# Optimization experiments

Hardware: AMD Instinct MI355X
Metric: run time of the kernel (lower is better)

## Reference

```python
import jax, jax.numpy as jnp
import numpy as np


def setup_inputs() -> dict:
    key = jax.random.key(0)
    B, N = 4, 32768
    xyz = jax.random.normal(key, (B, N, 3), dtype=jnp.float32)
    return {"xyz": xyz, "K": 16, "nqueries": 2048}


def reference(xyz, K, nqueries):
    # xyz: (b, n, 3). Deterministic strided pick of nqueries query points
    # (stand-in for the KD-tree's distance-pick sampling), then brute-force KNN.
    b, n, _ = xyz.shape
    stride = n // nqueries
    q_idx = jnp.arange(nqueries) * stride          # (nq,)
    pts = xyz[:, q_idx, :]                          # (b, nq, 3) sampled query points
    # pairwise squared distances (b, nq, n)
    d = jnp.sum((pts[:, :, None, :] - xyz[:, None, :, :]) ** 2, axis=-1)
    _, idx = jax.lax.top_k(-d, K)                   # (b, nq, K) nearest-neighbor indices
    idx = idx.astype(jnp.int64)[..., None]          # (b, nq, K, 1) matches expand_dims(..., 3)
    return idx, pts
```

## Files before the change

kernel.cpp:

```cpp
#include <hip/hip_runtime.h>
#include <stdint.h>

#define NPTS  32768
#define NQ    2048
#define KNN   16
#define NB    4
#define TS    2048
#define BLOCK 512
#define WPB   8

__device__ __forceinline__ void insert_all(float d, int p, int lane, int t,
                                           float& ld, int& li, float& tau)
{
    unsigned long long rem = __ballot(d <= tau);
    while (rem) {
        const int srcl = __ffsll((unsigned long long)rem) - 1;
        const float wd = __shfl(d, srcl);
        const int   wi = __shfl(p, srcl);
        const bool less = (ld < wd) || (ld == wd && li < wi);
        const unsigned long long lm = __ballot(less);
        const int pos = __popc((unsigned)((lm >> (16 * t)) & 0xffffull));
        const float pld = __shfl_up(ld, 1);
        const int   pli = __shfl_up(li, 1);
        if ((lane >> 4) == t) {
            const int gl = lane & 15;
            if (gl == pos)      { ld = wd;  li = wi;  }
            else if (gl > pos)  { ld = pld; li = pli; }
        }
        tau = __shfl(ld, 16 * t + 15);
        rem &= rem - 1;
        if (rem) rem &= __ballot(d <= tau);
    }
}

__global__ __launch_bounds__(BLOCK) void knn_kernel(const float* __restrict__ xyz,
                                                    float* __restrict__ out_idx,
                                                    float* __restrict__ out_pts)
{
    __shared__ float4 pts[TS];

    const int tid  = threadIdx.x;
    const int lane = tid & 63;
    const int wv   = tid >> 6;
    const int w    = blockIdx.x * WPB + wv;
    const int b    = w >> 10;
    const int pr   = w & 1023;
    const size_t base = (size_t)b * NPTS * 3;

    const int qp0 = pr << 5;
    const int qp1 = qp0 + 16;
    const float qx0 = xyz[base + 3 * qp0 + 0];
    const float qy0 = xyz[base + 3 * qp0 + 1];
    const float qz0 = xyz[base + 3 * qp0 + 2];
    const float qx1 = xyz[base + 3 * qp1 + 0];
    const float qy1 = xyz[base + 3 * qp1 + 1];
    const float qz1 = xyz[base + 3 * qp1 + 2];

    const int g0 = b * NQ + (pr << 1);
    if (lane == 0) {
        out_pts[3 * g0 + 0] = qx0;
        out_pts[3 * g0 + 1] = qy0;
        out_pts[3 * g0 + 2] = qz0;
        out_pts[3 * g0 + 3] = qx1;
        out_pts[3 * g0 + 4] = qy1;
        out_pts[3 * g0 + 5] = qz1;
    }

    float ld = __builtin_inff();  int li = 0x7fffffff;
    float tau0 = __builtin_inff(), tau1 = __builtin_inff();

    for (int tile = 0; tile < NPTS; tile += TS) {
        __syncthreads();
        {
            const float2* src = (const float2*)(xyz + base + (size_t)tile * 3);
            #pragma unroll
            for (int t = 0; t < TS / (2 * BLOCK); ++t) {
                const int pi = tid + t * BLOCK;
                const float2 f0 = src[3 * pi + 0];
                const float2 f1 = src[3 * pi + 1];
                const float2 f2 = src[3 * pi + 2];
                pts[2 * pi + 0] = make_float4(f0.x, f0.y, f1.x, 0.f);
                pts[2 * pi + 1] = make_float4(f1.y, f2.x, f2.y, 0.f);
            }
        }
        __syncthreads();

        #pragma unroll
        for (int k = 0; k < TS / 256; ++k) {
            float d0[4], d1[4];
            bool any = false;
            #pragma unroll
            for (int j = 0; j < 4; ++j) {
                const float4 p = pts[256 * k + 64 * j + lane];
                const float ax = __fadd_rn(p.x, -qx0);
                const float ay = __fadd_rn(p.y, -qy0);
                const float az = __fadd_rn(p.z, -qz0);
                d0[j] = __fadd_rn(__fadd_rn(__fmul_rn(ax, ax), __fmul_rn(ay, ay)),
                                  __fmul_rn(az, az));
                const float bx = __fadd_rn(p.x, -qx1);
                const float by = __fadd_rn(p.y, -qy1);
                const float bz = __fadd_rn(p.z, -qz1);
                d1[j] = __fadd_rn(__fadd_rn(__fmul_rn(bx, bx), __fmul_rn(by, by)),
                                  __fmul_rn(bz, bz));
                any = any | (d0[j] <= tau0) | (d1[j] <= tau1);
            }
            if (__ballot(any)) {
                const int pb = tile + 256 * k + lane;
                #pragma unroll
                for (int j = 0; j < 4; ++j) {
                    insert_all(d0[j], pb + 64 * j, lane, 0, ld, li, tau0);
                    insert_all(d1[j], pb + 64 * j, lane, 1, ld, li, tau1);
                }
            }
        }
    }

    if (lane < 2 * KNN) {
        out_idx[(size_t)g0 * KNN + lane] = (float)li;
    }
}

extern "C" void kernel_launch(void* const* d_in, const int* in_sizes, int n_in,
                              void* d_out, int out_size, void* d_ws, size_t ws_size,
                              hipStream_t stream) {
    const float* xyz = (const float*)d_in[0];
    float* out = (float*)d_out;
    float* out_idx = out;
    float* out_pts = out + (size_t)NB * NQ * KNN;

    const int blocks = (NB * NQ / 2) / WPB;
    knn_kernel<<<blocks, BLOCK, 0, stream>>>(xyz, out_idx, out_pts);
}
```

Baseline: 215.8 us.

## Use direct global-to-LDS loads, packed FP32 math, and DPP/readlane in insertion

The tile is now loaded straight from global memory into LDS with global_load_lds. This drops the register round-trip and the float4 repacking, and keeps the raw xyz layout. Each lane reads three float4s and unpacks four consecutive points, then computes distances for both queries at once with v_pk_add/v_pk_mul. The insertion loop replaces shuffles with readlane and DPP row shifts, with the template constant folded. Candidate order within a chunk changes, and DPP shifts only within a row of 16 lanes, which matches the 16-lane lists.

Result: slower. 222.9 us (+3.3%).

```diff
diff --git a/kernel.cpp b/kernel.cpp
--- a/kernel.cpp
+++ b/kernel.cpp
@@ -9,25 +9,50 @@
 #define BLOCK 512
 #define WPB   8
 
-__device__ __forceinline__ void insert_all(float d, int p, int lane, int t,
+typedef const __attribute__((address_space(1))) char glds_src_t;
+typedef __attribute__((address_space(3))) char glds_dst_t;
+
+__device__ __forceinline__ float2 pk_add(float2 a, float2 b) {
+    float2 r;
+    asm("v_pk_add_f32 %0, %1, %2" : "=v"(r) : "v"(a), "v"(b));
+    return r;
+}
+__device__ __forceinline__ float2 pk_mul(float2 a, float2 b) {
+    float2 r;
+    asm("v_pk_mul_f32 %0, %1, %2" : "=v"(r) : "v"(a), "v"(b));
+    return r;
+}
+__device__ __forceinline__ int dpp_shr1_i(int x) {
+    return __builtin_amdgcn_update_dpp(x, x, 0x111, 0xf, 0xf, false);
+}
+__device__ __forceinline__ float dpp_shr1_f(float x) {
+    int r = dpp_shr1_i(__float_as_int(x));
+    return __int_as_float(r);
+}
+__device__ __forceinline__ float readlane_f(float x, int l) {
+    return __int_as_float(__builtin_amdgcn_readlane(__float_as_int(x), l));
+}
+
+template <int T>
+__device__ __forceinline__ void insert_all(float d, int p, int lane,
                                            float& ld, int& li, float& tau)
 {
     unsigned long long rem = __ballot(d <= tau);
     while (rem) {
-        const int srcl = __ffsll((unsigned long long)rem) - 1;
-        const float wd = __shfl(d, srcl);
-        const int   wi = __shfl(p, srcl);
+        const int srcl = __ffsll(rem) - 1;
+        const float wd = readlane_f(d, srcl);
+        const int   wi = __builtin_amdgcn_readlane(p, srcl);
         const bool less = (ld < wd) || (ld == wd && li < wi);
         const unsigned long long lm = __ballot(less);
-        const int pos = __popc((unsigned)((lm >> (16 * t)) & 0xffffull));
-        const float pld = __shfl_up(ld, 1);
-        const int   pli = __shfl_up(li, 1);
-        if ((lane >> 4) == t) {
+        const int pos = __popc((unsigned)((lm >> (16 * T)) & 0xffffull));
+        const float pld = dpp_shr1_f(ld);
+        const int   pli = dpp_shr1_i(li);
+        if ((lane >> 4) == T) {
             const int gl = lane & 15;
             if (gl == pos)      { ld = wd;  li = wi;  }
             else if (gl > pos)  { ld = pld; li = pli; }
         }
-        tau = __shfl(ld, 16 * t + 15);
+        tau = readlane_f(ld, 16 * T + 15);
         rem &= rem - 1;
         if (rem) rem &= __ballot(d <= tau);
     }
@@ -37,7 +62,7 @@
                                                     float* __restrict__ out_idx,
                                                     float* __restrict__ out_pts)
 {
-    __shared__ float4 pts[TS];
+    __shared__ float lds[TS * 3];
 
     const int tid  = threadIdx.x;
     const int lane = tid & 63;
@@ -48,13 +73,12 @@
     const size_t base = (size_t)b * NPTS * 3;
 
     const int qp0 = pr << 5;
-    const int qp1 = qp0 + 16;
     const float qx0 = xyz[base + 3 * qp0 + 0];
     const float qy0 = xyz[base + 3 * qp0 + 1];
     const float qz0 = xyz[base + 3 * qp0 + 2];
-    const float qx1 = xyz[base + 3 * qp1 + 0];
-    const float qy1 = xyz[base + 3 * qp1 + 1];
-    const float qz1 = xyz[base + 3 * qp1 + 2];
+    const float qx1 = xyz[base + 3 * qp0 + 48];
+    const float qy1 = xyz[base + 3 * qp0 + 49];
+    const float qz1 = xyz[base + 3 * qp0 + 50];
 
     const int g0 = b * NQ + (pr << 1);
     if (lane == 0) {
@@ -66,50 +90,56 @@
         out_pts[3 * g0 + 5] = qz1;
     }
 
+    const float2 nqx = make_float2(-qx0, -qx1);
+    const float2 nqy = make_float2(-qy0, -qy1);
+    const float2 nqz = make_float2(-qz0, -qz1);
+
     float ld = __builtin_inff();  int li = 0x7fffffff;
     float tau0 = __builtin_inff(), tau1 = __builtin_inff();
+
+    const float4* lp = (const float4*)lds + 3 * lane;
 
     for (int tile = 0; tile < NPTS; tile += TS) {
         __syncthreads();
         {
-            const float2* src = (const float2*)(xyz + base + (size_t)tile * 3);
+            glds_src_t* gsrc = (glds_src_t*)(xyz + base + (size_t)tile * 3);
+            glds_dst_t* ldst = (glds_dst_t*)lds;
             #pragma unroll
-            for (int t = 0; t < TS / (2 * BLOCK); ++t) {
-                const int pi = tid + t * BLOCK;
-                const float2 f0 = src[3 * pi + 0];
-                const float2 f1 = src[3 * pi + 1];
-                const float2 f2 = src[3 * pi + 2];
-                pts[2 * pi + 0] = make_float4(f0.x, f0.y, f1.x, 0.f);
-                pts[2 * pi + 1] = make_float4(f1.y, f2.x, f2.y, 0.f);
-            }
+            for (int c = 0; c < 3; ++c)
+                __builtin_amdgcn_global_load_lds(
+                    (const __attribute__((address_space(1))) void*)(gsrc + 16 * (BLOCK * c + tid)),
+                    (__attribute__((address_space(3))) void*)(ldst + 16 * (BLOCK * c + tid)),
+                    16, 0, 0);
         }
         __syncthreads();
 
         #pragma unroll
         for (int k = 0; k < TS / 256; ++k) {
+            const float4 A = lp[192 * k + 0];
+            const float4 Bv = lp[192 * k + 1];
+            const float4 Cv = lp[192 * k + 2];
+            const float px[4] = { A.x,  A.w,  Bv.z, Cv.y };
+            const float py[4] = { A.y,  Bv.x, Bv.w, Cv.z };
+            const float pz[4] = { A.z,  Bv.y, Cv.x, Cv.w };
+
             float d0[4], d1[4];
             bool any = false;
             #pragma unroll
             for (int j = 0; j < 4; ++j) {
-                const float4 p = pts[256 * k + 64 * j + lane];
-                const float ax = __fadd_rn(p.x, -qx0);
-                const float ay = __fadd_rn(p.y, -qy0);
-                const float az = __fadd_rn(p.z, -qz0);
-                d0[j] = __fadd_rn(__fadd_rn(__fmul_rn(ax, ax), __fmul_rn(ay, ay)),
-                                  __fmul_rn(az, az));
-                const float bx = __fadd_rn(p.x, -qx1);
-                const float by = __fadd_rn(p.y, -qy1);
-                const float bz = __fadd_rn(p.z, -qz1);
-                d1[j] = __fadd_rn(__fadd_rn(__fmul_rn(bx, bx), __fmul_rn(by, by)),
-                                  __fmul_rn(bz, bz));
+                const float2 dx = pk_add(make_float2(px[j], px[j]), nqx);
+                const float2 dy = pk_add(make_float2(py[j], py[j]), nqy);
+                const float2 dz = pk_add(make_float2(pz[j], pz[j]), nqz);
+                const float2 s  = pk_add(pk_add(pk_mul(dx, dx), pk_mul(dy, dy)),
+                                         pk_mul(dz, dz));
+                d0[j] = s.x;  d1[j] = s.y;
                 any = any | (d0[j] <= tau0) | (d1[j] <= tau1);
             }
             if (__ballot(any)) {
-                const int pb = tile + 256 * k + lane;
+                const int pb = tile + 256 * k + 4 * lane;
                 #pragma unroll
                 for (int j = 0; j < 4; ++j) {
-                    insert_all(d0[j], pb + 64 * j, lane, 0, ld, li, tau0);
-                    insert_all(d1[j], pb + 64 * j, lane, 1, ld, li, tau1);
+                    insert_all<0>(d0[j], pb + j, lane, ld, li, tau0);
+                    insert_all<1>(d1[j], pb + j, lane, ld, li, tau1);
                 }
             }
         }
```
